# Kernel tuning notes

Hardware: AMD Instinct MI355X
Metric: run time of the kernel (lower is better)

Reference implementation:

```python
import jax, jax.numpy as jnp
import numpy as np

# dims: batch, seq (<=300 due to tril buffer), raw embed, model dim (hardcoded 300), experts, heads, head_size
B, T, D_IN, D, E, H, HS = 64, 300, 768, 300, 8, 4, 16
TOP_K = E // 2


def setup_inputs() -> dict:
    key = jax.random.key(0)
    ks = jax.random.split(key, 10)
    f = lambda k, s, sc: jax.random.normal(k, s, jnp.float32) * sc
    return {
        "x": jax.random.normal(ks[0], (B, T, D_IN), jnp.float32),
        "wh_bias": jnp.zeros((D_IN,), jnp.float32),
        "wh_W": f(ks[1], (D, D_IN), 0.02),              # WhitenLayer linear (no bias)
        "Wq": f(ks[2], (H, HS, D), 0.05),                # stacked per-head query weights
        "Wk": f(ks[3], (H, HS, D), 0.05),
        "Wv": f(ks[4], (H, HS, D), 0.05),
        "proj_W": f(ks[5], (D, H * HS), 0.05),
        "proj_b": jnp.zeros((D,), jnp.float32),
        "exp_W1": f(ks[6], (E, 2 * D, D), (2.0 / (2 * D)) ** 0.5),  # kaiming fan_out
        "exp_b1": jnp.zeros((E, 2 * D), jnp.float32),
        "exp_W2": f(ks[7], (E, D, 2 * D), (2.0 / D) ** 0.5),
        "exp_b2": jnp.zeros((E, D), jnp.float32),
        "w_gate": f(ks[8], (D, E), 0.02),
    }


def reference(x, wh_bias, wh_W, Wq, Wk, Wv, proj_W, proj_b,
              exp_W1, exp_b1, exp_W2, exp_b2, w_gate):
    # WhitenLayer: lin(x - bias)  (dropout identity in eval)
    xw = jnp.einsum('btd,od->bto', x - wh_bias, wh_W)          # [B,T,D]

    # MultiHeadAttention (causal, scale = C**-0.5 with C = D = 300)
    q = jnp.einsum('btd,hkd->bhtk', xw, Wq)
    k = jnp.einsum('btd,hkd->bhtk', xw, Wk)
    v = jnp.einsum('btd,hkd->bhtk', xw, Wv)
    wei = jnp.einsum('bhtk,bhsk->bhts', q, k) * (D ** -0.5)
    tril = jnp.tril(jnp.ones((T, T), bool))
    wei = jax.nn.softmax(jnp.where(tril, wei, -jnp.inf), axis=-1)
    att = jnp.einsum('bhts,bhsk->bthk', wei, v).reshape(x.shape[0], T, H * HS)
    xa = att @ proj_W.T + proj_b                               # [B,T,D]

    # noisy_top_k_gating in eval mode (no noise); masked dispatch == dense weighted sum
    logits = xa @ w_gate                                       # [B,T,E]
    topv, topi = jax.lax.top_k(logits, TOP_K)
    sel = jax.nn.one_hot(topi, E, dtype=bool).any(axis=-2)     # [B,T,E] top-k mask
    sparse = jnp.where(sel, logits, -jnp.inf)
    gprob = jax.nn.softmax(sparse, axis=-1)                    # zero on non-selected

    # all experts applied densely (forward also recomputes them all anyway)
    h = jax.nn.relu(jnp.einsum('btd,ehd->bteh', xa, exp_W1) + exp_b1)
    eo = jnp.einsum('bteh,eoh->bteo', h, exp_W2) + exp_b2      # [B,T,E,D]

    gates = jnp.einsum('bte,bteo->bto', gprob, eo)             # dispatched mixture [B,T,D]
    # forward: (gates.unsqueeze(-2) * expert_outputs).sum(-2) == gates * sum_e expert_e
    return gates * eo.sum(axis=-2)
```

## Files before the change

### kernel.cpp

```cpp
#include <hip/hip_runtime.h>
#include <cstdint>
#include <cstddef>

#define B_   64
#define T_   300
#define DIN_ 768
#define D_   300
#define E_   8
#define NTOK (B_*T_)

typedef __attribute__((ext_vector_type(8))) short bf8_t;
typedef __attribute__((ext_vector_type(4))) float f4_t;

__device__ __forceinline__ unsigned short f2bf(float v) {
  union { float f; unsigned u; } a; a.f = v;
  unsigned r = a.u + 0x7fff + ((a.u >> 16) & 1);
  return (unsigned short)(r >> 16);
}
__device__ __forceinline__ float bf2f(unsigned short s) {
  union { float f; unsigned u; } a; a.u = ((unsigned)s) << 16; return a.f;
}
__device__ __forceinline__ void split3(float v, unsigned short& p0,
                                       unsigned short& p1, unsigned short& p2) {
  p0 = f2bf(v);
  float r1 = v - bf2f(p0);
  p1 = f2bf(r1);
  float r2 = r1 - bf2f(p1);
  p2 = f2bf(r2);
}
__device__ __forceinline__ void split2(float v, unsigned short& p0,
                                       unsigned short& p1) {
  p0 = f2bf(v);
  p1 = f2bf(v - bf2f(p0));
}

__device__ __forceinline__ void gld16(const unsigned short* g, unsigned short* l) {
  __builtin_amdgcn_global_load_lds(
      (const __attribute__((address_space(1))) unsigned int*)g,
      (__attribute__((address_space(3))) unsigned int*)l, 16, 0, 0);
}

__global__ void biasproj_kernel(const float* __restrict__ wh_bias,
                                const float* __restrict__ wh_W,
                                float* __restrict__ bp) {
  int o = blockIdx.x * blockDim.x + threadIdx.x;
  if (o >= D_) return;
  float acc = 0.f;
  const float* row = wh_W + (size_t)o * DIN_;
  for (int d = 0; d < DIN_; ++d) acc += wh_bias[d] * row[d];
  bp[o] = -acc;
}

__global__ void split_pad(const float* __restrict__ src, unsigned short* __restrict__ dst,
                          int rows, int K, int Kp, size_t planeStride, int np) {
  int n = rows * Kp;
  for (int i = blockIdx.x * blockDim.x + threadIdx.x; i < n; i += gridDim.x * blockDim.x) {
    int r = i / Kp, c = i % Kp;
    unsigned short p0 = 0, p1 = 0, p2 = 0;
    if (c < K) split3(src[(size_t)r * K + c], p0, p1, p2);
    dst[i] = p0;
    dst[planeStride + i] = p1;
    if (np == 3) dst[2 * planeStride + i] = p2;
  }
}

template<int AFP, int EPI, int JN, int WM, int NP, int NPO, int SWZ>
__global__ __launch_bounds__(WM * 64) void mfma_gen(
    const void* __restrict__ Av, size_t aPStride, int ldA,
    const unsigned short* __restrict__ Bg, size_t bPStride,
    const float* __restrict__ bias, float* __restrict__ C,
    unsigned short* __restrict__ Po, size_t poStride, int ldPo,
    float* __restrict__ gsum, float* __restrict__ esum,
    const float* __restrict__ gate,
    int M, int N, int K) {
  constexpr int TILE_M = WM * 32;
  constexpr int BROWS  = JN * 32;
  constexpr int APB    = TILE_M * 64;
  constexpr int BPB    = BROWS * 64;
  constexpr int AINSTS = NP * APB / 1024;
  constexpr int BINSTS = NP * BPB / 1024;
  static_assert(!AFP || NP == 3, "AFP path writes 3 planes");
  __shared__ unsigned short Ap[NP][TILE_M * 32];
  __shared__ unsigned short Bp[NP][BROWS * 32];
  const int tid = threadIdx.x;
  int bxv = blockIdx.x, byv = blockIdx.y;
  if constexpr (SWZ) {
    const int nx  = gridDim.x;
    const int nwg = nx * gridDim.y;
    const int id  = byv * nx + bxv;
    const int xcd = id & 7, idx = id >> 3;
    const int q = nwg >> 3, r = nwg & 7;
    const int nid = (xcd < r) ? (xcd * (q + 1) + idx)
                              : (r * (q + 1) + (xcd - r) * q + idx);
    bxv = nid % nx;
    byv = nid / nx;
  }
  const int bm = byv * TILE_M, bn = bxv * BROWS;
  const int widx = tid >> 6;
  const int wr = (widx >> 1) * 64;
  const int wc = (widx & 1) * (JN * 16);
  const int lane = tid & 63;
  const int lr = lane & 15;
  const int kg = lane >> 4;
  const int sw = (lr >> 1) & 3;
  const int Kp = (K + 31) & ~31;
  const int arow = tid >> 1, ahalf = (tid & 1) * 16;
  const int asw = (arow >> 1) & 3;

  f4_t acc[4][JN];
  #pragma unroll
  for (int i = 0; i < 4; ++i)
    #pragma unroll
    for (int j = 0; j < JN; ++j) acc[i][j] = (f4_t){0.f, 0.f, 0.f, 0.f};

  for (int k0 = 0; k0 < Kp; k0 += 32) {
    for (int q = widx; q < BINSTS; q += WM) {
      const int f   = q * 1024 + lane * 16;
      const int pp  = f / BPB;
      const int rem = f % BPB;
      const int row = rem >> 6;
      const int cl  = ((rem >> 4) & 3) ^ ((row >> 1) & 3);
      int brow = bn + row; if (brow >= N) brow = N - 1;
      gld16(Bg + (size_t)pp * bPStride + (size_t)brow * Kp + k0 + cl * 8,
            (unsigned short*)Bp + q * 512);
    }
    if constexpr (AFP) {
      const float* Arow = (const float*)Av + (size_t)(bm + arow) * ldA + k0 + ahalf;
      #pragma unroll
      for (int u = 0; u < 4; ++u) {
        float4 qv = *(const float4*)&Arow[u * 4];
        float vv[4] = {qv.x, qv.y, qv.z, qv.w};
        unsigned short s0[4], s1[4], s2[4];
        #pragma unroll
        for (int w = 0; w < 4; ++w) split3(vv[w], s0[w], s1[w], s2[w]);
        const int k  = ahalf + u * 4;
        const int so = arow * 32 + (((k >> 3) ^ asw) << 3) + (k & 7);
        *(unsigned*)&Ap[0][so]     = (unsigned)s0[0] | ((unsigned)s0[1] << 16);
        *(unsigned*)&Ap[0][so + 2] = (unsigned)s0[2] | ((unsigned)s0[3] << 16);
        *(unsigned*)&Ap[1][so]     = (unsigned)s1[0] | ((unsigned)s1[1] << 16);
        *(unsigned*)&Ap[1][so + 2] = (unsigned)s1[2] | ((unsigned)s1[3] << 16);
        *(unsigned*)&Ap[2][so]     = (unsigned)s2[0] | ((unsigned)s2[1] << 16);
        *(unsigned*)&Ap[2][so + 2] = (unsigned)s2[2] | ((unsigned)s2[3] << 16);
      }
    } else {
      for (int q = widx; q < AINSTS; q += WM) {
        const int f   = q * 1024 + lane * 16;
        const int pp  = f / APB;
        const int rem = f % APB;
        const int row = rem >> 6;
        const int cl  = ((rem >> 4) & 3) ^ ((row >> 1) & 3);
        gld16((const unsigned short*)Av + (size_t)pp * aPStride +
                  (size_t)(bm + row) * Kp + k0 + cl * 8,
              (unsigned short*)Ap + q * 512);
      }
    }
    __syncthreads();
    bf8_t a[4][NP], b[JN][NP];
    #pragma unroll
    for (int i = 0; i < 4; ++i)
      #pragma unroll
      for (int p = 0; p < NP; ++p)
        a[i][p] = *(const bf8_t*)&Ap[p][(wr + i * 16 + lr) * 32 + ((kg ^ sw) << 3)];
    #pragma unroll
    for (int j = 0; j < JN; ++j)
      #pragma unroll
      for (int p = 0; p < NP; ++p)
        b[j][p] = *(const bf8_t*)&Bp[p][(wc + j * 16 + lr) * 32 + ((kg ^ sw) << 3)];
    #pragma unroll
    for (int i = 0; i < 4; ++i)
      #pragma unroll
      for (int j = 0; j < JN; ++j) {
        f4_t c = acc[i][j];
        if constexpr (NP == 3) {
          c = __builtin_amdgcn_mfma_f32_16x16x32_bf16(a[i][2], b[j][0], c, 0, 0, 0);
          c = __builtin_amdgcn_mfma_f32_16x16x32_bf16(a[i][1], b[j][1], c, 0, 0, 0);
          c = __builtin_amdgcn_mfma_f32_16x16x32_bf16(a[i][0], b[j][2], c, 0, 0, 0);
          c = __builtin_amdgcn_mfma_f32_16x16x32_bf16(a[i][1], b[j][0], c, 0, 0, 0);
          c = __builtin_amdgcn_mfma_f32_16x16x32_bf16(a[i][0], b[j][1], c, 0, 0, 0);
          c = __builtin_amdgcn_mfma_f32_16x16x32_bf16(a[i][0], b[j][0], c, 0, 0, 0);
        } else {
          c = __builtin_amdgcn_mfma_f32_16x16x32_bf16(a[i][1], b[j][0], c, 0, 0, 0);
          c = __builtin_amdgcn_mfma_f32_16x16x32_bf16(a[i][0], b[j][1], c, 0, 0, 0);
          c = __builtin_amdgcn_mfma_f32_16x16x32_bf16(a[i][0], b[j][0], c, 0, 0, 0);
        }
        acc[i][j] = c;
      }
    __syncthreads();
  }
  #pragma unroll
  for (int i = 0; i < 4; ++i) {
    #pragma unroll
    for (int r = 0; r < 4; ++r) {
      const int row = bm + wr + i * 16 + kg * 4 + r;
      float g = 0.f;
      if constexpr (EPI >= 2 && EPI <= 4) g = gate[(size_t)row * E_];
      #pragma unroll
      for (int j = 0; j < JN; ++j) {
        const int col = bn + wc + j * 16 + lr;
        float v = acc[i][j][r];
        if constexpr (EPI == 0) {
          if (col < N) {
            if (bias) v += bias[col];
            C[(size_t)row * N + col] = v;
          }
        } else if constexpr (EPI == 1 || EPI == 5 || EPI == 6) {
          if (col < ldPo) {
            unsigned short p0 = 0, p1 = 0, p2 = 0;
            if (col < N) {
              v += bias[col];
              if constexpr (EPI == 1) v = fmaxf(v, 0.f);
              if constexpr (EPI == 6) C[(size_t)row * N + col] = v;
              if constexpr (NPO == 3) split3(v, p0, p1, p2);
              else                    split2(v, p0, p1);
            }
            size_t o = (size_t)row * ldPo + col;
            Po[o] = p0;
            Po[poStride + o] = p1;
            if constexpr (NPO == 3) Po[2 * poStride + o] = p2;
          }
        } else {
          if (col < N) {
            float eo = v + bias[col];
            size_t idx = (size_t)row * N + col;
            if constexpr (EPI == 2) {
              gsum[idx] = g * eo;
              esum[idx] = eo;
            } else if constexpr (EPI == 3) {
              gsum[idx] += g * eo;
              esum[idx] += eo;
            } else {
              float gs = gsum[idx] + g * eo;
              float es = esum[idx] + eo;
              C[idx] = gs * es;
            }
          }
        }
      }
    }
  }
}

__global__ __launch_bounds__(64) void attn_kernel(
    const float* __restrict__ qkv, float* __restrict__ attout) {
  const int bt = blockIdx.x;
  const int b = bt / T_, t = bt % T_;
  const int lane = threadIdx.x;
  const int h = lane >> 4, li = lane & 15;
  __shared__ float p[4][304];
  const float scale = rsqrtf((float)D_);
  const float* qrow = qkv + (size_t)bt * 192 + h * 16;
  const float4 q0 = *(const float4*)(qrow);
  const float4 q1 = *(const float4*)(qrow + 4);
  const float4 q2 = *(const float4*)(qrow + 8);
  const float4 q3 = *(const float4*)(qrow + 12);
  const float* kb0 = qkv + (size_t)b * T_ * 192 + 64 + h * 16;
  float mmax = -1e30f;
  for (int s = li; s <= t; s += 16) {
    const float* kr = kb0 + (size_t)s * 192;
    float4 k0 = *(const float4*)(kr);
    float4 k1 = *(const float4*)(kr + 4);
    float4 k2 = *(const float4*)(kr + 8);
    float4 k3 = *(const float4*)(kr + 12);
    float acc = q0.x * k0.x + q0.y * k0.y + q0.z * k0.z + q0.w * k0.w;
    acc += q1.x * k1.x + q1.y * k1.y + q1.z * k1.z + q1.w * k1.w;
    acc += q2.x * k2.x + q2.y * k2.y + q2.z * k2.z + q2.w * k2.w;
    acc += q3.x * k3.x + q3.y * k3.y + q3.z * k3.z + q3.w * k3.w;
    acc *= scale;
    p[h][s] = acc;
    mmax = fmaxf(mmax, acc);
  }
  #pragma unroll
  for (int m = 8; m >= 1; m >>= 1) mmax = fmaxf(mmax, __shfl_xor(mmax, m, 16));
  float lsum = 0.f;
  for (int s = li; s <= t; s += 16) {
    float e = __expf(p[h][s] - mmax);
    p[h][s] = e;
    lsum += e;
  }
  #pragma unroll
  for (int m = 8; m >= 1; m >>= 1) lsum += __shfl_xor(lsum, m, 16);
  const float inv = 1.0f / lsum;
  const float* vcol = qkv + (size_t)b * T_ * 192 + 128 + h * 16 + li;
  float o0 = 0.f, o1 = 0.f, o2 = 0.f, o3 = 0.f;
  const int s4 = (t + 1) & ~3;
  int s = 0;
  for (; s < s4; s += 4) {
    float4 pw = *(const float4*)&p[h][s];
    o0 += pw.x * vcol[(size_t)s * 192];
    o1 += pw.y * vcol[(size_t)(s + 1) * 192];
    o2 += pw.z * vcol[(size_t)(s + 2) * 192];
    o3 += pw.w * vcol[(size_t)(s + 3) * 192];
  }
  for (; s <= t; ++s) o0 += p[h][s] * vcol[(size_t)s * 192];
  attout[(size_t)bt * 192 + lane] = ((o0 + o1) + (o2 + o3)) * inv;
}

__global__ void logits_kernel(const float* __restrict__ xa,
                              const float* __restrict__ w_gate,
                              float* __restrict__ logits) {
  int idx = blockIdx.x * blockDim.x + threadIdx.x;
  if (idx >= NTOK * E_) return;
  int n = idx >> 3, e = idx & 7;
  const float* xr = xa + (size_t)n * D_;
  float acc = 0.f;
  for (int d = 0; d < D_; ++d) acc += xr[d] * w_gate[(size_t)d * E_ + e];
  logits[idx] = acc;
}

__global__ void gate_kernel(const float* __restrict__ logits,
                            float* __restrict__ gprob) {
  int n = blockIdx.x * blockDim.x + threadIdx.x;
  if (n >= NTOK) return;
  float l[E_];
  #pragma unroll
  for (int e = 0; e < E_; ++e) l[e] = logits[(size_t)n * E_ + e];
  bool sel[E_] = {false, false, false, false, false, false, false, false};
  for (int kk = 0; kk < E_ / 2; ++kk) {
    int bi = -1; float bv = -1e38f;
    #pragma unroll
    for (int e = 0; e < E_; ++e)
      if (!sel[e] && l[e] > bv) { bv = l[e]; bi = e; }
    sel[bi] = true;
  }
  float mx = -1e38f;
  #pragma unroll
  for (int e = 0; e < E_; ++e) if (sel[e]) mx = fmaxf(mx, l[e]);
  float s = 0.f, pp[E_];
  #pragma unroll
  for (int e = 0; e < E_; ++e) {
    pp[e] = sel[e] ? __expf(l[e] - mx) : 0.f;
    s += pp[e];
  }
  float inv = 1.0f / s;
  #pragma unroll
  for (int e = 0; e < E_; ++e) gprob[(size_t)n * E_ + e] = pp[e] * inv;
}

extern "C" void kernel_launch(void* const* d_in, const int* in_sizes, int n_in,
                              void* d_out, int out_size, void* d_ws, size_t ws_size,
                              hipStream_t stream) {
  const float* x       = (const float*)d_in[0];
  const float* wh_bias = (const float*)d_in[1];
  const float* wh_W    = (const float*)d_in[2];
  const float* Wq      = (const float*)d_in[3];
  const float* Wk      = (const float*)d_in[4];
  const float* Wv      = (const float*)d_in[5];
  const float* proj_W  = (const float*)d_in[6];
  const float* proj_b  = (const float*)d_in[7];
  const float* exp_W1  = (const float*)d_in[8];
  const float* exp_b1  = (const float*)d_in[9];
  const float* exp_W2  = (const float*)d_in[10];
  const float* exp_b2  = (const float*)d_in[11];
  const float* w_gate  = (const float*)d_in[12];
  (void)in_sizes; (void)n_in; (void)out_size;

  char* ws = (char*)d_ws;
  size_t off = 0;
  auto alloc = [&](size_t bytes) {
    void* p = ws + off; off = (off + bytes + 255) & ~(size_t)255; return p;
  };
  typedef unsigned short us;
  float* bp    = (float*)alloc(300 * 4);
  us* whp      = (us*)alloc((size_t)3 * 300 * 768 * 2);
  us* qkvp     = (us*)alloc((size_t)2 * 192 * 320 * 2);
  us* projp    = (us*)alloc((size_t)3 * 300 * 64 * 2);
  us* w1p      = (us*)alloc((size_t)2 * 4800 * 320 * 2);
  us* w2p      = (us*)alloc(((size_t)2 * 2400 * 608 + 64 * 608) * 2);
  float* gprob = (float*)alloc((size_t)NTOK * E_ * 4);
  us* xwreg    = (us*)alloc((size_t)2 * NTOK * 320 * 2);
  float* qkvb  = (float*)alloc((size_t)NTOK * 192 * 4);
  us* xap      = (us*)alloc((size_t)2 * NTOK * 320 * 2);

  float* xa = (float*)xwreg;

  const size_t hplBytes  = (size_t)2 * NTOK * 608 * 2;
  const size_t esumBytes = (size_t)NTOK * 300 * 4;
  int CHe;
  us* hpl;
  float* esum;
  if (off + hplBytes + esumBytes <= ws_size) {
    hpl  = (us*)alloc(hplBytes);
    esum = (float*)alloc(esumBytes);
    CHe  = NTOK;
  } else {
    hpl  = xwreg;
    esum = qkvb;
    CHe  = 9600;
  }

  biasproj_kernel<<<2, 256, 0, stream>>>(wh_bias, wh_W, bp);
  auto SP = [&](const float* s, us* dbase, int rows, int K, int Kp, size_t pstr, int np) {
    int n = rows * Kp;
    int g = (n + 255) / 256; if (g > 4096) g = 4096;
    split_pad<<<g, 256, 0, stream>>>(s, dbase, rows, K, Kp, pstr, np);
  };
  SP(wh_W,   whp,              300,  768, 768, (size_t)300 * 768, 3);
  SP(Wq,     qkvp,             64,   300, 320, (size_t)192 * 320, 2);
  SP(Wk,     qkvp + 64 * 320,  64,   300, 320, (size_t)192 * 320, 2);
  SP(Wv,     qkvp + 128 * 320, 64,   300, 320, (size_t)192 * 320, 2);
  SP(proj_W, projp,            300,  64,  64,  (size_t)300 * 64, 3);
  SP(exp_W1, w1p,              4800, 300, 320, (size_t)4800 * 320, 2);
  SP(exp_W2, w2p,              2400, 600, 608, (size_t)2400 * 608, 2);

  {
    dim3 g(5, NTOK / 128);
    mfma_gen<1, 5, 2, 4, 3, 2, 0><<<g, 256, 0, stream>>>(
        x, 0, DIN_, whp, (size_t)300 * 768, bp, nullptr,
        xwreg, (size_t)NTOK * 320, 320, nullptr, nullptr, nullptr,
        NTOK, D_, DIN_);
  }
  {
    dim3 g(3, NTOK / 128);
    mfma_gen<0, 0, 2, 4, 2, 2, 0><<<g, 256, 0, stream>>>(
        xwreg, (size_t)NTOK * 320, 0, qkvp, (size_t)192 * 320, nullptr, qkvb,
        nullptr, 0, 0, nullptr, nullptr, nullptr,
        NTOK, 192, D_);
  }
  attn_kernel<<<NTOK, 64, 0, stream>>>(qkvb, qkvb);

  {
    dim3 g(5, NTOK / 128);
    mfma_gen<1, 6, 2, 4, 3, 2, 0><<<g, 256, 0, stream>>>(
        qkvb, 0, 192, projp, (size_t)300 * 64, proj_b, xa,
        xap, (size_t)NTOK * 320, 320, nullptr, nullptr, nullptr,
        NTOK, D_, 64);
  }
  logits_kernel<<<(NTOK * E_ + 255) / 256, 256, 0, stream>>>(xa, w_gate, gprob);
  gate_kernel<<<(NTOK + 255) / 256, 256, 0, stream>>>(gprob, gprob);

  for (int c = 0; c < NTOK / CHe; ++c) {
    const int tok0 = c * CHe;
    float* gsum = (float*)d_out + (size_t)tok0 * D_;
    dim3 g1(5, CHe / 128);
    dim3 g2(5, CHe / 128);
    for (int e = 0; e < E_; ++e) {
      const us* w1e = w1p + (size_t)e * 600 * 320;
      const us* w2e = w2p + (size_t)e * 300 * 608;
      const float* bb1 = exp_b1 + (size_t)e * 600;
      const float* bb2 = exp_b2 + (size_t)e * D_;
      const float* gate = gprob + (size_t)tok0 * E_ + e;
      mfma_gen<0, 1, 4, 4, 2, 2, 1><<<g1, 256, 0, stream>>>(
          xap + (size_t)tok0 * 320, (size_t)NTOK * 320, 0,
          w1e, (size_t)4800 * 320, bb1, nullptr,
          hpl, (size_t)CHe * 608, 608, nullptr, nullptr, nullptr,
          CHe, 600, D_);
      if (e == 0)
        mfma_gen<0, 2, 2, 4, 2, 2, 1><<<g2, 256, 0, stream>>>(
            hpl, (size_t)CHe * 608, 0, w2e, (size_t)2400 * 608, bb2, nullptr,
            nullptr, 0, 0, gsum, esum, gate, CHe, D_, 600);
      else if (e < E_ - 1)
        mfma_gen<0, 3, 2, 4, 2, 2, 1><<<g2, 256, 0, stream>>>(
            hpl, (size_t)CHe * 608, 0, w2e, (size_t)2400 * 608, bb2, nullptr,
            nullptr, 0, 0, gsum, esum, gate, CHe, D_, 600);
      else
        mfma_gen<0, 4, 2, 4, 2, 2, 1><<<g2, 256, 0, stream>>>(
            hpl, (size_t)CHe * 608, 0, w2e, (size_t)2400 * 608, bb2,
            (float*)d_out + (size_t)tok0 * D_,
            nullptr, 0, 0, gsum, esum, gate, CHe, D_, 600);
    }
  }
}
```

Measured before the change: 992.5 us.

## Overlap next-tile staging with MFMA compute and pre-split x into bf16 planes

The GEMM main loop now reads the current tile's fragments into registers, syncs, and then issues global-to-LDS loads for the next K tile before running the MFMAs, so memory latency overlaps with compute. When the workspace is large enough, the input x is also pre-split into three bf16 planes by a separate kernel, so the whitening GEMM can use the bf16 load path instead of splitting fp32 inline. The last template argument also changes from 0 to 1 for several launches. The pre-split adds an extra pass that writes and reads about three times x in bf16, and it shares a workspace region with hpl/esum, so correctness depends on that aliasing being safe.

```diff
diff --git a/kernel.cpp b/kernel.cpp
--- a/kernel.cpp
+++ b/kernel.cpp
@@ -107,13 +107,7 @@
   const int arow = tid >> 1, ahalf = (tid & 1) * 16;
   const int asw = (arow >> 1) & 3;
 
-  f4_t acc[4][JN];
-  #pragma unroll
-  for (int i = 0; i < 4; ++i)
-    #pragma unroll
-    for (int j = 0; j < JN; ++j) acc[i][j] = (f4_t){0.f, 0.f, 0.f, 0.f};
-
-  for (int k0 = 0; k0 < Kp; k0 += 32) {
+  auto stageB = [&](int k0) {
     for (int q = widx; q < BINSTS; q += WM) {
       const int f   = q * 1024 + lane * 16;
       const int pp  = f / BPB;
@@ -124,6 +118,8 @@
       gld16(Bg + (size_t)pp * bPStride + (size_t)brow * Kp + k0 + cl * 8,
             (unsigned short*)Bp + q * 512);
     }
+  };
+  auto stageA = [&](int k0) {
     if constexpr (AFP) {
       const float* Arow = (const float*)Av + (size_t)(bm + arow) * ldA + k0 + ahalf;
       #pragma unroll
@@ -154,7 +150,17 @@
               (unsigned short*)Ap + q * 512);
       }
     }
-    __syncthreads();
+  };
+
+  f4_t acc[4][JN];
+  #pragma unroll
+  for (int i = 0; i < 4; ++i)
+    #pragma unroll
+    for (int j = 0; j < JN; ++j) acc[i][j] = (f4_t){0.f, 0.f, 0.f, 0.f};
+
+  stageB(0); stageA(0);
+  __syncthreads();
+  for (int k0 = 0; k0 < Kp; k0 += 32) {
     bf8_t a[4][NP], b[JN][NP];
     #pragma unroll
     for (int i = 0; i < 4; ++i)
@@ -166,6 +172,8 @@
       #pragma unroll
       for (int p = 0; p < NP; ++p)
         b[j][p] = *(const bf8_t*)&Bp[p][(wc + j * 16 + lr) * 32 + ((kg ^ sw) << 3)];
+    __syncthreads();
+    if (k0 + 32 < Kp) { stageB(k0 + 32); stageA(k0 + 32); }
     #pragma unroll
     for (int i = 0; i < 4; ++i)
       #pragma unroll
@@ -373,12 +381,24 @@
 
   float* xa = (float*)xwreg;
 
+  const size_t xp3Bytes  = (size_t)3 * NTOK * DIN_ * 2;
   const size_t hplBytes  = (size_t)2 * NTOK * 608 * 2;
   const size_t esumBytes = (size_t)NTOK * 300 * 4;
+  const size_t hplAl = (hplBytes + 255) & ~(size_t)255;
   int CHe;
   us* hpl;
   float* esum;
-  if (off + hplBytes + esumBytes <= ws_size) {
+  us* xp3 = nullptr;
+  bool preX = false;
+  if (off + xp3Bytes <= ws_size) {
+    char* region = ws + off;
+    off += (xp3Bytes + 255) & ~(size_t)255;
+    xp3  = (us*)region;
+    hpl  = (us*)region;
+    esum = (float*)(region + hplAl);
+    CHe  = NTOK;
+    preX = true;
+  } else if (off + hplBytes + esumBytes <= ws_size) {
     hpl  = (us*)alloc(hplBytes);
     esum = (float*)alloc(esumBytes);
     CHe  = NTOK;
@@ -402,16 +422,23 @@
   SP(exp_W1, w1p,              4800, 300, 320, (size_t)4800 * 320, 2);
   SP(exp_W2, w2p,              2400, 600, 608, (size_t)2400 * 608, 2);
 
-  {
+  if (preX) {
+    SP(x, xp3, NTOK, DIN_, DIN_, (size_t)NTOK * DIN_, 3);
     dim3 g(5, NTOK / 128);
-    mfma_gen<1, 5, 2, 4, 3, 2, 0><<<g, 256, 0, stream>>>(
+    mfma_gen<0, 5, 2, 4, 3, 2, 1><<<g, 256, 0, stream>>>(
+        xp3, (size_t)NTOK * DIN_, 0, whp, (size_t)300 * 768, bp, nullptr,
+        xwreg, (size_t)NTOK * 320, 320, nullptr, nullptr, nullptr,
+        NTOK, D_, DIN_);
+  } else {
+    dim3 g(5, NTOK / 128);
+    mfma_gen<1, 5, 2, 4, 3, 2, 1><<<g, 256, 0, stream>>>(
         x, 0, DIN_, whp, (size_t)300 * 768, bp, nullptr,
         xwreg, (size_t)NTOK * 320, 320, nullptr, nullptr, nullptr,
         NTOK, D_, DIN_);
   }
   {
     dim3 g(3, NTOK / 128);
-    mfma_gen<0, 0, 2, 4, 2, 2, 0><<<g, 256, 0, stream>>>(
+    mfma_gen<0, 0, 2, 4, 2, 2, 1><<<g, 256, 0, stream>>>(
         xwreg, (size_t)NTOK * 320, 0, qkvp, (size_t)192 * 320, nullptr, qkvb,
         nullptr, 0, 0, nullptr, nullptr, nullptr,
         NTOK, 192, D_);
@@ -420,7 +447,7 @@
 
   {
     dim3 g(5, NTOK / 128);
-    mfma_gen<1, 6, 2, 4, 3, 2, 0><<<g, 256, 0, stream>>>(
+    mfma_gen<1, 6, 2, 4, 3, 2, 1><<<g, 256, 0, stream>>>(
         qkvb, 0, 192, projp, (size_t)300 * 64, proj_b, xa,
         xap, (size_t)NTOK * 320, 320, nullptr, nullptr, nullptr,
         NTOK, D_, 64);
```

New measurement: 988.2 us. Within noise of the previous version (-0.4%).
